# Kernel optimization log

Measured on AMD Instinct MI355X. Metric: run time of the kernel, lower is better.

## Reference

```python
import jax, jax.numpy as jnp
import numpy as np

H = 768; IDX_D = 64; K = 10; R = 12; READ_K = 100; MD = 64; WK = 100; INTER = 3072
SIZES = (100, 1000, 10000, 50000); N = SIZES[-1]; DEPTH = len(SIZES)
B = 4; E = 128
SQ_IDX = np.float32(np.sqrt(IDX_D)); SQ_MD = np.float32(np.sqrt(MD))


def setup_inputs():
    ks = jax.random.split(jax.random.key(0), 16)
    d = {}
    d['elem_hiddens'] = jax.random.normal(ks[0], (B, E, H), jnp.float32)
    d['elems_to_elems'] = 0.05 * jax.random.normal(ks[1], (B, R, E, E), jnp.float32)
    d['Wq_idx'] = jax.random.normal(ks[2], (H, DEPTH * IDX_D), jnp.float32) / np.float32(np.sqrt(H))
    d['bq_idx'] = jnp.zeros((DEPTH * IDX_D,), jnp.float32)
    d['key0'] = 0.01 * jax.random.normal(ks[3], (SIZES[0], IDX_D), jnp.float32)
    d['key1'] = 0.01 * jax.random.normal(ks[4], (SIZES[0], SIZES[1] // SIZES[0], IDX_D), jnp.float32)
    d['key2'] = 0.01 * jax.random.normal(ks[5], (SIZES[1], SIZES[2] // SIZES[1], IDX_D), jnp.float32)
    d['key3'] = 0.01 * jax.random.normal(ks[6], (SIZES[2], SIZES[3] // SIZES[2], IDX_D), jnp.float32)
    d['memory_keys'] = 0.01 * jax.random.normal(ks[7], (R, N, MD), jnp.float32)
    d['memory_values'] = 0.01 * jax.random.normal(ks[8], (R, N, MD), jnp.float32)
    d['wiring_weights'] = jax.random.normal(ks[9], (R, N, WK), jnp.float32)
    d['Wq_mha'] = jax.random.normal(ks[10], (H, R * MD), jnp.float32) / np.float32(np.sqrt(H))
    d['bq_mha'] = jnp.zeros((R * MD,), jnp.float32)
    d['W1'] = jax.random.normal(ks[11], (R * MD, INTER), jnp.float32) / np.float32(np.sqrt(R * MD))
    d['b1'] = jnp.zeros((INTER,), jnp.float32)
    d['W2'] = jax.random.normal(ks[12], (INTER, H), jnp.float32) / np.float32(np.sqrt(INTER))
    d['b2'] = jnp.zeros((H,), jnp.float32)
    d['ln_g'] = jnp.ones((H,), jnp.float32)
    d['ln_b'] = jnp.zeros((H,), jnp.float32)
    d['wiring_edges'] = jax.random.randint(ks[13], (R, N, WK), 0, N, jnp.int32)
    return d


def _indexer(x, Wq, bq, keys):
    # hierarchical product-key top-k retrieval; ind holds node ids at each level
    q = (x @ Wq + bq).reshape(x.shape[:-1] + (DEPTH, IDX_D))
    attn = jax.nn.softmax(jnp.einsum('bed,nd->ben', q[..., 0, :], keys[0]) / SQ_IDX, axis=-1)
    val, ind = jax.lax.top_k(attn, K)
    val = val / val.sum(-1, keepdims=True)
    for i in range(1, DEPTH):
        branch = SIZES[i] // SIZES[i - 1]
        kk = keys[i][ind]  # [B,E,K,branch,D] gather children of surviving nodes
        s = jax.nn.softmax(jnp.einsum('bed,bekcd->bekc', q[..., i, :], kk) / SQ_IDX, axis=-1)
        a = (val[..., None] * s).reshape(x.shape[:-1] + (K * branch,))
        val, f = jax.lax.top_k(a, K)
        ind = jnp.take_along_axis(ind, f // branch, axis=-1) * branch + f % branch
        val = val / val.sum(-1, keepdims=True)
    return val, ind  # [B,E,K] weights, [B,E,K] node ids in [0,N)


def reference(elem_hiddens, elems_to_elems, Wq_idx, bq_idx, key0, key1, key2, key3, memory_keys, memory_values, wiring_weights, Wq_mha, bq_mha, W1, b1, W2, b2, ln_g, ln_b, wiring_edges):
    e2n_val, e2n_ind = _indexer(elem_hiddens, Wq_idx, bq_idx, (key0, key1, key2, key3))
    rows = jnp.arange(B * E)[:, None]
    write_loss = jnp.float32(0.0)
    mem_keys_l, mem_vals_l = [], []
    for r in range(R):
        # sparse-sparse matmul e2n @ n2n realized as gather + scatter-add (coalesces dups like spspmm)
        nbr = wiring_edges[r][e2n_ind]  # [B,E,K,WK]
        w = wiring_weights[r][e2n_ind]  # [B,E,K,WK]
        cand_val = (e2n_val[..., None] * w).reshape(B * E, K * WK)
        cand_col = nbr.reshape(B * E, K * WK)
        e22n = jnp.zeros((B * E, N), jnp.float32).at[rows, cand_col].add(cand_val).reshape(B, E, N)
        # e222e[b,i,j] = sum_a e2n_val[b,j,a] * e22n[b,i,e2n_ind[b,j,a]] (batch-block-diagonal spspmm)
        g = jnp.take_along_axis(e22n[:, :, None, :], e2n_ind[:, None, :, :], axis=-1)  # [B,Ei,Ej,K]
        e222e = jnp.einsum('bijk,bjk->bij', g, e2n_val)
        write_loss = write_loss + jnp.mean((e222e - elems_to_elems[:, r]) ** 2)
        _, top_ind = jax.lax.top_k(e22n, READ_K)  # sparse_topk per row (>=~500 positive nnz per row)
        mem_keys_l += [memory_keys[r][e2n_ind], memory_keys[r][top_ind]]
        mem_vals_l += [memory_values[r][e2n_ind], memory_values[r][top_ind]]
    slots = K + READ_K
    mem_keys = jnp.concatenate(mem_keys_l, axis=2).reshape(B, E, R, slots, MD)
    mem_vals = jnp.concatenate(mem_vals_l, axis=2).reshape(B, E, R, slots, MD)
    # multi-head read; note: original scores queries against VALUES (not keys)
    qh = (elem_hiddens @ Wq_mha + bq_mha).reshape(B, E, R, MD)
    attn = jax.nn.softmax(jnp.einsum('berd,bersd->bers', qh, mem_vals) / SQ_MD, axis=-1)
    attd = jnp.einsum('bers,bersd->berd', attn, mem_vals).reshape(B, E, R * MD)
    h = jax.nn.gelu(attd @ W1 + b1, approximate=False) @ W2 + b2
    mu = h.mean(-1, keepdims=True)
    out = (h - mu) / jnp.sqrt(((h - mu) ** 2).mean(-1, keepdims=True) + 1e-5) * ln_g + ln_b
    return out, write_loss
```

## Files before the change

kernel.cpp:

```cpp
#include <hip/hip_runtime.h>
#include <hip/hip_bf16.h>
#include <cfloat>
#include <cmath>

#define H_DIM 768
#define IDX_D 64
#define KTOP 10
#define R_HEADS 12
#define READ_K 100
#define MD 64
#define WK 100
#define INTER 3072
#define N_NODES 50000
#define B_SZ 4
#define E_SZ 128
#define BE 512
#define SLOTS 110
#define HASH_SZ 2048
#define HASH_MASK 2047

__global__ void zero_loss_kernel(float* p) {
    if (threadIdx.x == 0 && blockIdx.x == 0) *p = 0.f;
}
__global__ void write_loss_kernel(const float* p, float* out) {
    if (threadIdx.x == 0 && blockIdx.x == 0) out[0] = *p / 65536.f;
}

__global__ __launch_bounds__(256) void gemm_kernel(
    const float* __restrict__ A, const float* __restrict__ Bm,
    const float* __restrict__ bias, float* __restrict__ C,
    int M, int N, int K, int act)
{
    __shared__ float As[2][16][65];
    __shared__ float Bs[2][16][65];
    const int tid = threadIdx.x;
    const int tx = tid & 15, ty = tid >> 4;
    const int m0 = blockIdx.y * 64, n0 = blockIdx.x * 64;

    const int aty = tid >> 4, atx = tid & 15;
    const int bky = tid >> 6, bnx = tid & 63;

    float acc[4][4] = {};
    float av[4], bv[4];

    auto stage = [&](int k0) {
        #pragma unroll
        for (int j = 0; j < 4; ++j)
            av[j] = A[(size_t)(m0 + aty + 16 * j) * K + k0 + atx];
        #pragma unroll
        for (int j = 0; j < 4; ++j)
            bv[j] = Bm[(size_t)(k0 + bky + 4 * j) * N + n0 + bnx];
    };
    auto commit = [&](int buf) {
        #pragma unroll
        for (int j = 0; j < 4; ++j) As[buf][atx][aty + 16 * j] = av[j];
        #pragma unroll
        for (int j = 0; j < 4; ++j) Bs[buf][bky + 4 * j][bnx] = bv[j];
    };
    auto compute = [&](int buf) {
        #pragma unroll
        for (int kk = 0; kk < 16; ++kk) {
            float a4[4], b4[4];
            #pragma unroll
            for (int u = 0; u < 4; ++u) a4[u] = As[buf][kk][ty * 4 + u];
            #pragma unroll
            for (int v = 0; v < 4; ++v) b4[v] = Bs[buf][kk][tx * 4 + v];
            #pragma unroll
            for (int u = 0; u < 4; ++u)
                #pragma unroll
                for (int v = 0; v < 4; ++v) acc[u][v] += a4[u] * b4[v];
        }
    };

    stage(0);
    commit(0);
    __syncthreads();
    int buf = 0;
    for (int k0 = 16; k0 < K; k0 += 16) {
        stage(k0);
        compute(buf);
        commit(buf ^ 1);
        __syncthreads();
        buf ^= 1;
    }
    compute(buf);

    #pragma unroll
    for (int u = 0; u < 4; ++u) {
        int m = m0 + ty * 4 + u;
        #pragma unroll
        for (int v = 0; v < 4; ++v) {
            int n = n0 + tx * 4 + v;
            float x = acc[u][v] + bias[n];
            if (act) x = 0.5f * x * (1.f + erff(x * 0.70710678118654752f));
            C[(size_t)m * N + n] = x;
        }
    }
}

typedef short bf16x8 __attribute__((ext_vector_type(8)));
typedef float f32x4 __attribute__((ext_vector_type(4)));
typedef unsigned int u32x4 __attribute__((ext_vector_type(4)));

__device__ inline unsigned f2bf(float x) {
    unsigned u = __float_as_uint(x);
    return (u + 0x7FFFu + ((u >> 16) & 1u)) >> 16;
}
__device__ inline float bfval(unsigned b) { return __uint_as_float(b << 16); }

__global__ __launch_bounds__(256) void gemm_mfma_kernel(
    const float* __restrict__ A, const float* __restrict__ Bm,
    const float* __restrict__ bias, float* __restrict__ C,
    int M, int N, int Kc, int lda, int act)
{
    __shared__ __align__(16) unsigned int lds[2][4][2048];

    const int tid = threadIdx.x;
    const int lane = tid & 63;
    const int w = tid >> 6, wr = w >> 1, wc = w & 1;
    const int m0 = blockIdx.y * 128, n0 = blockIdx.x * 128;
    const int kbase = blockIdx.z * Kc;
    float* __restrict__ Cp = C + (size_t)blockIdx.z * M * N;

    f32x4 acc[4][4] = {};
    unsigned apk[2][8];
    unsigned bpk[2][8];

    auto stage = [&](int k0) {
        #pragma unroll
        for (int it = 0; it < 8; ++it) {
            int idx = it * 256 + tid;
            int r = idx >> 4, p = idx & 15;
            const float2 v = *(const float2*)(A + (size_t)(m0 + r) * lda + kbase + k0 + 2 * p);
            unsigned h0 = f2bf(v.x), h1 = f2bf(v.y);
            apk[0][it] = h0 | (h1 << 16);
            apk[1][it] = f2bf(v.x - bfval(h0)) | (f2bf(v.y - bfval(h1)) << 16);
        }
        #pragma unroll
        for (int it = 0; it < 4; ++it) {
            int idx = it * 256 + tid;
            int cp = idx & 63, kp = idx >> 6;
            const float* bp = Bm + (size_t)(kbase + k0 + 2 * kp) * N + n0 + 2 * cp;
            const float2 e = *(const float2*)bp;
            const float2 o = *(const float2*)(bp + N);
            unsigned he0 = f2bf(e.x), ho0 = f2bf(o.x);
            unsigned he1 = f2bf(e.y), ho1 = f2bf(o.y);
            bpk[0][it * 2 + 0] = he0 | (ho0 << 16);
            bpk[1][it * 2 + 0] = f2bf(e.x - bfval(he0)) | (f2bf(o.x - bfval(ho0)) << 16);
            bpk[0][it * 2 + 1] = he1 | (ho1 << 16);
            bpk[1][it * 2 + 1] = f2bf(e.y - bfval(he1)) | (f2bf(o.y - bfval(ho1)) << 16);
        }
    };

    auto commit = [&](int buf) {
        #pragma unroll
        for (int it = 0; it < 8; ++it) {
            int idx = it * 256 + tid;
            int r = idx >> 4, p = idx & 15;
            int off = ((r >> 4) * 256) + ((p >> 2) * 64) + ((r & 15) * 4) + (p & 3);
            lds[buf][0][off] = apk[0][it];
            lds[buf][1][off] = apk[1][it];
        }
        #pragma unroll
        for (int it = 0; it < 4; ++it) {
            int idx = it * 256 + tid;
            int cp = idx & 63, kp = idx >> 6;
            int c = 2 * cp, g = kp >> 2, jj = kp & 3;
            int off0 = ((c >> 4) * 256) + (g * 64) + ((c & 15) * 4) + jj;
            lds[buf][2][off0]     = bpk[0][it * 2 + 0];
            lds[buf][3][off0]     = bpk[1][it * 2 + 0];
            lds[buf][2][off0 + 4] = bpk[0][it * 2 + 1];
            lds[buf][3][off0 + 4] = bpk[1][it * 2 + 1];
        }
    };

    auto ldfrag = [&](const unsigned* p) -> bf16x8 {
        return __builtin_bit_cast(bf16x8, *(const u32x4*)p);
    };

    auto compute = [&](int buf) {
        bf16x8 ah[4], al[4], bh[4], bl[4];
        #pragma unroll
        for (int mt = 0; mt < 4; ++mt) {
            int sub = wr * 4 + mt;
            ah[mt] = ldfrag(&lds[buf][0][sub * 256 + lane * 4]);
            al[mt] = ldfrag(&lds[buf][1][sub * 256 + lane * 4]);
        }
        #pragma unroll
        for (int nt = 0; nt < 4; ++nt) {
            int sub = wc * 4 + nt;
            bh[nt] = ldfrag(&lds[buf][2][sub * 256 + lane * 4]);
            bl[nt] = ldfrag(&lds[buf][3][sub * 256 + lane * 4]);
        }
        #pragma unroll
        for (int mt = 0; mt < 4; ++mt)
            #pragma unroll
            for (int nt = 0; nt < 4; ++nt) {
                acc[mt][nt] = __builtin_amdgcn_mfma_f32_16x16x32_bf16(ah[mt], bh[nt], acc[mt][nt], 0, 0, 0);
                acc[mt][nt] = __builtin_amdgcn_mfma_f32_16x16x32_bf16(ah[mt], bl[nt], acc[mt][nt], 0, 0, 0);
                acc[mt][nt] = __builtin_amdgcn_mfma_f32_16x16x32_bf16(al[mt], bh[nt], acc[mt][nt], 0, 0, 0);
            }
    };

    stage(0);
    commit(0);
    __syncthreads();
    int buf = 0;
    for (int k0 = 32; k0 < Kc; k0 += 32) {
        stage(k0);
        compute(buf);
        commit(buf ^ 1);
        __syncthreads();
        buf ^= 1;
    }
    compute(buf);

    const int rb0 = (lane >> 4) * 4, cc = lane & 15;
    #pragma unroll
    for (int mt = 0; mt < 4; ++mt) {
        #pragma unroll
        for (int nt = 0; nt < 4; ++nt) {
            int col = n0 + wc * 64 + nt * 16 + cc;
            int row = m0 + wr * 64 + mt * 16 + rb0;
            float b = bias ? bias[col] : 0.f;
            #pragma unroll
            for (int reg = 0; reg < 4; ++reg) {
                float x = acc[mt][nt][reg] + b;
                if (act) x = 0.5f * x * (1.f + erff(x * 0.70710678118654752f));
                Cp[(size_t)(row + reg) * N + col] = x;
            }
        }
    }
}

__device__ inline void wave_topk10(volatile float* a, int cnt,
                                   float* vnew, int* inew, int t)
{
    for (int iter = 0; iter < 10; ++iter) {
        float bv = -FLT_MAX;
        int bi = 0x7fffffff;
        for (int n = t; n < cnt; n += 64) {
            float v = a[n];
            if (v > bv) { bv = v; bi = n; }
        }
        #pragma unroll
        for (int off = 32; off; off >>= 1) {
            float ov = __shfl_xor(bv, off, 64);
            int   oi = __shfl_xor(bi, off, 64);
            if (ov > bv || (ov == bv && oi < bi)) { bv = ov; bi = oi; }
        }
        if (t == 0) { vnew[iter] = bv; inew[iter] = bi; a[bi] = -FLT_MAX; }
        __syncthreads();
    }
}

__global__ __launch_bounds__(64) void indexer_kernel(
    const float* __restrict__ qidx,
    const float* __restrict__ key0,
    const float* __restrict__ key1,
    const float* __restrict__ key2,
    const float* __restrict__ key3,
    float* __restrict__ e2n_val,
    int* __restrict__ e2n_ind)
{
    const int be = blockIdx.x;
    const int t = threadIdx.x;
    __shared__ float q[256];
    __shared__ float sraw[100];
    __shared__ float a[100];
    __shared__ float vnew[10]; __shared__ int inew[10];
    __shared__ float vcur[10]; __shared__ int icur[10];
    __shared__ float km[10], ks[10];

    for (int idx = t; idx < 256; idx += 64) q[idx] = qidx[(size_t)be * 256 + idx];
    __syncthreads();

    for (int n = t; n < 100; n += 64) {
        float dot = 0.f;
        const float* kp = key0 + (size_t)n * 64;
        #pragma unroll 8
        for (int d = 0; d < 64; ++d) dot += q[d] * kp[d];
        sraw[n] = dot * 0.125f;
    }
    __syncthreads();
    float lm = -FLT_MAX;
    for (int n = t; n < 100; n += 64) lm = fmaxf(lm, sraw[n]);
    #pragma unroll
    for (int off = 32; off; off >>= 1) lm = fmaxf(lm, __shfl_xor(lm, off, 64));
    float lsum = 0.f;
    for (int n = t; n < 100; n += 64) { float e = expf(sraw[n] - lm); a[n] = e; lsum += e; }
    #pragma unroll
    for (int off = 32; off; off >>= 1) lsum += __shfl_xor(lsum, off, 64);
    __syncthreads();
    for (int n = t; n < 100; n += 64) a[n] /= lsum;
    __syncthreads();
    wave_topk10(a, 100, vnew, inew, t);
    if (t == 0) {
        float s = 0.f;
        for (int u = 0; u < 10; ++u) s += vnew[u];
        for (int u = 0; u < 10; ++u) { vcur[u] = vnew[u] / s; icur[u] = inew[u]; }
    }
    __syncthreads();

    for (int lvl = 1; lvl < 4; ++lvl) {
        const int br = (lvl < 3) ? 10 : 5;
        const float* kb = (lvl == 1) ? key1 : ((lvl == 2) ? key2 : key3);
        const int cnt = 10 * br;
        const float* qv = q + lvl * 64;
        for (int c = t; c < cnt; c += 64) {
            int k = c / br, cc = c - k * br;
            const float* kp = kb + ((size_t)icur[k] * br + cc) * 64;
            float dot = 0.f;
            #pragma unroll 8
            for (int d = 0; d < 64; ++d) dot += qv[d] * kp[d];
            sraw[c] = dot * 0.125f;
        }
        __syncthreads();
        if (t < 10) {
            float m = -FLT_MAX;
            for (int cc = 0; cc < br; ++cc) m = fmaxf(m, sraw[t * br + cc]);
            float s = 0.f;
            for (int cc = 0; cc < br; ++cc) s += expf(sraw[t * br + cc] - m);
            km[t] = m; ks[t] = s;
        }
        __syncthreads();
        for (int c = t; c < cnt; c += 64) {
            int k = c / br;
            a[c] = vcur[k] * expf(sraw[c] - km[k]) / ks[k];
        }
        __syncthreads();
        wave_topk10(a, cnt, vnew, inew, t);
        if (t == 0) {
            float s = 0.f;
            for (int u = 0; u < 10; ++u) s += vnew[u];
            int ni[10]; float nv[10];
            for (int u = 0; u < 10; ++u) {
                int f = inew[u];
                ni[u] = icur[f / br] * br + (f % br);
                nv[u] = vnew[u] / s;
            }
            for (int u = 0; u < 10; ++u) { icur[u] = ni[u]; vcur[u] = nv[u]; }
        }
        __syncthreads();
    }
    if (t < 10) {
        e2n_val[(size_t)be * 10 + t] = vcur[t];
        e2n_ind[(size_t)be * 10 + t] = icur[t];
    }
}

__global__ __launch_bounds__(256) void scatter_loss_topk_kernel(
    const int* __restrict__ e2n_ind,
    const float* __restrict__ e2n_val,
    const int* __restrict__ edges,
    const float* __restrict__ wts,
    const float* __restrict__ e2e,
    int* __restrict__ top_ind,
    float* __restrict__ loss_acc)
{
    __shared__ int   hkey[HASH_SZ];
    __shared__ float hval[HASH_SZ];
    __shared__ int   pool[2560];
    __shared__ float red[256];
    __shared__ int   chunkSuf[256];
    __shared__ int   s_t, s_above, s_cntA, s_cntB;

    const int blk = blockIdx.x;
    const int r = blk >> 9;
    const int be = blk & 511;
    const int b = be >> 7, i = be & 127;
    const int tid = threadIdx.x;

    int* s_ind = pool;
    float* s_val = (float*)(pool + 1280);

    for (int idx = tid; idx < E_SZ * KTOP; idx += 256) {
        s_ind[idx] = e2n_ind[(size_t)b * E_SZ * KTOP + idx];
        s_val[idx] = e2n_val[(size_t)b * E_SZ * KTOP + idx];
    }
    for (int idx = tid; idx < HASH_SZ; idx += 256) { hkey[idx] = -1; hval[idx] = 0.f; }
    if (tid == 0) { s_t = -1; s_above = 0; s_cntA = 0; s_cntB = 0; }
    __syncthreads();

    const size_t rbase = (size_t)r * N_NODES * WK;
    for (int c = tid; c < KTOP * WK; c += 256) {
        int k = c / WK, wk = c - k * WK;
        int node = s_ind[i * KTOP + k];
        float v0 = s_val[i * KTOP + k];
        size_t off = rbase + (size_t)node * WK + wk;
        int col = edges[off];
        float v = v0 * wts[off];
        unsigned h = ((unsigned)col * 2654435761u) >> 21;
        for (;;) {
            int old = atomicCAS(&hkey[h], -1, col);
            if (old == -1 || old == col) { atomicAdd(&hval[h], v); break; }
            h = (h + 1) & HASH_MASK;
        }
    }
    __syncthreads();

    {
        const int j = tid & 127, half = tid >> 7;
        float acc = 0.f;
        #pragma unroll
        for (int k = half * 5; k < half * 5 + 5; ++k) {
            int col = s_ind[j * KTOP + k];
            float vv = s_val[j * KTOP + k];
            unsigned h = ((unsigned)col * 2654435761u) >> 21;
            float g = 0.f;
            for (;;) {
                int kk = hkey[h];
                if (kk == col) { g = hval[h]; break; }
                if (kk == -1) break;
                h = (h + 1) & HASH_MASK;
            }
            acc += vv * g;
        }
        red[tid] = acc;
        __syncthreads();
        float sq = 0.f;
        if (tid < 128) {
            float tot = red[tid] + red[tid + 128];
            float d = tot - e2e[(((size_t)b * R_HEADS + r) * E_SZ + i) * E_SZ + tid];
            sq = d * d;
        }
        __syncthreads();
        red[tid] = sq;
        __syncthreads();
        for (int off = 128; off; off >>= 1) {
            if (tid < off) red[tid] += red[tid + off];
            __syncthreads();
        }
        if (tid == 0) atomicAdd(loss_acc, red[0]);
    }
    __syncthreads();

    int* hist = pool;
    for (int idx = tid; idx < HASH_SZ; idx += 256) hist[idx] = 0;
    __syncthreads();
    for (int idx = tid; idx < HASH_SZ; idx += 256) {
        float v = hval[idx];
        if (hkey[idx] != -1 && v > 0.f)
            atomicAdd(&hist[(__float_as_uint(v) >> 20) & 0x7FF], 1);
    }
    __syncthreads();
    {
        int csum = 0;
        #pragma unroll
        for (int bb = 0; bb < 8; ++bb) csum += hist[tid * 8 + bb];
        chunkSuf[tid] = csum;
    }
    __syncthreads();
    if (tid == 0) {
        int suf = 0;
        for (int c = 255; c >= 0; --c) { int t0 = chunkSuf[c]; chunkSuf[c] = suf; suf += t0; }
    }
    __syncthreads();
    {
        int cum = chunkSuf[tid];
        for (int bb = tid * 8 + 7; bb >= tid * 8; --bb) {
            int h = hist[bb];
            if (cum < READ_K && cum + h >= READ_K) { s_t = bb; s_above = cum; }
            cum += h;
        }
    }
    __syncthreads();
    const int tbin = s_t;

    int* bcol = pool;
    float* bval = (float*)(pool + 1024);
    __syncthreads();
    int* outp = top_ind + ((size_t)be * R_HEADS + r) * READ_K;
    for (int idx = tid; idx < HASH_SZ; idx += 256) {
        float v = hval[idx];
        if (hkey[idx] == -1 || v <= 0.f) continue;
        int bin = (__float_as_uint(v) >> 20) & 0x7FF;
        if (bin > tbin) {
            int p = atomicAdd(&s_cntA, 1);
            if (p < READ_K) outp[p] = hkey[idx];
        } else if (bin == tbin) {
            int p = atomicAdd(&s_cntB, 1);
            bcol[p] = hkey[idx]; bval[p] = v;
        }
    }
    __syncthreads();
    const int above = s_cntA;
    const int m = s_cntB;
    int rem = READ_K - above;
    if (rem >= m) {
        for (int idx = tid; idx < m; idx += 256) outp[above + idx] = bcol[idx];
        for (int idx = above + m + tid; idx < READ_K; idx += 256) outp[idx] = 0;
    } else if (tid < 64) {
        volatile float* bv_ = bval;
        for (int it = 0; it < rem; ++it) {
            float bvx = -FLT_MAX; int bi = -1;
            for (int n = tid; n < m; n += 64) {
                float v = bv_[n];
                if (v > bvx) { bvx = v; bi = n; }
            }
            #pragma unroll
            for (int off = 32; off; off >>= 1) {
                float ov = __shfl_xor(bvx, off, 64);
                int   oi = __shfl_xor(bi, off, 64);
                if (ov > bvx) { bvx = ov; bi = oi; }
            }
            if (tid == 0) { outp[above + it] = bcol[bi]; bv_[bi] = -FLT_MAX; }
        }
    }
}

__global__ __launch_bounds__(128) void attn_kernel(
    const float* __restrict__ qh,
    const int* __restrict__ e2n_ind,
    const int* __restrict__ top_ind,
    const float* __restrict__ memv,
    float* __restrict__ attd)
{
    __shared__ float vv[SLOTS * 65];
    __shared__ int slots[SLOTS];
    __shared__ float qv[64];
    __shared__ float sc[SLOTS];
    __shared__ float red[128];

    const int blk = blockIdx.x;
    const int r = blk >> 9, be = blk & 511;
    const int tid = threadIdx.x;

    if (tid < KTOP) slots[tid] = e2n_ind[(size_t)be * KTOP + tid];
    else if (tid < SLOTS) slots[tid] = top_ind[((size_t)be * R_HEADS + r) * READ_K + (tid - KTOP)];
    if (tid < 64) qv[tid] = qh[(size_t)be * H_DIM + r * 64 + tid];
    __syncthreads();

    const size_t rb = (size_t)r * N_NODES * 64;
    for (int idx = tid; idx < SLOTS * 64; idx += 128) {
        int s = idx >> 6, d = idx & 63;
        vv[s * 65 + d] = memv[rb + (size_t)slots[s] * 64 + d];
    }
    __syncthreads();

    if (tid < SLOTS) {
        float dot = 0.f;
        const float* vp = vv + tid * 65;
        #pragma unroll 8
        for (int d = 0; d < 64; ++d) dot += qv[d] * vp[d];
        sc[tid] = dot * 0.125f;
    }
    __syncthreads();

    red[tid] = (tid < SLOTS) ? sc[tid] : -FLT_MAX;
    __syncthreads();
    for (int off = 64; off; off >>= 1) {
        if (tid < off) red[tid] = fmaxf(red[tid], red[tid + off]);
        __syncthreads();
    }
    float m = red[0];
    __syncthreads();
    float e = (tid < SLOTS) ? expf(sc[tid] - m) : 0.f;
    red[tid] = e;
    __syncthreads();
    for (int off = 64; off; off >>= 1) {
        if (tid < off) red[tid] += red[tid + off];
        __syncthreads();
    }
    float sum = red[0];
    if (tid < SLOTS) sc[tid] = e / sum;
    __syncthreads();

    {
        const int d = tid & 63;
        const int s0 = (tid >> 6) * 55;
        float acc = 0.f;
        for (int s = s0; s < s0 + 55; ++s) acc += sc[s] * vv[s * 65 + d];
        red[tid] = acc;
        __syncthreads();
        if (tid < 64)
            attd[(size_t)be * H_DIM + r * 64 + tid] = red[tid] + red[tid + 64];
    }
}

__global__ __launch_bounds__(256) void ln_kernel(
    const float* __restrict__ hp,
    const float* __restrict__ b2,
    const float* __restrict__ g,
    const float* __restrict__ bta, float* __restrict__ out)
{
    const int be = blockIdx.x, tid = threadIdx.x;
    __shared__ float red[256];
    const size_t st = (size_t)BE * H_DIM;
    const size_t base = (size_t)be * 768;
    float x0 = b2[tid], x1 = b2[tid + 256], x2 = b2[tid + 512];
    #pragma unroll
    for (int s = 0; s < 4; ++s) {
        x0 += hp[s * st + base + tid];
        x1 += hp[s * st + base + 256 + tid];
        x2 += hp[s * st + base + 512 + tid];
    }
    red[tid] = x0 + x1 + x2;
    __syncthreads();
    for (int off = 128; off; off >>= 1) { if (tid < off) red[tid] += red[tid + off]; __syncthreads(); }
    const float mu = red[0] * (1.f / 768.f);
    __syncthreads();
    const float d0 = x0 - mu, d1 = x1 - mu, d2 = x2 - mu;
    red[tid] = d0 * d0 + d1 * d1 + d2 * d2;
    __syncthreads();
    for (int off = 128; off; off >>= 1) { if (tid < off) red[tid] += red[tid + off]; __syncthreads(); }
    const float rstd = rsqrtf(red[0] * (1.f / 768.f) + 1e-5f);
    out[(size_t)be * 768 + tid]       = d0 * rstd * g[tid]       + bta[tid];
    out[(size_t)be * 768 + 256 + tid] = d1 * rstd * g[tid + 256] + bta[tid + 256];
    out[(size_t)be * 768 + 512 + tid] = d2 * rstd * g[tid + 512] + bta[tid + 512];
}

extern "C" void kernel_launch(void* const* d_in, const int* in_sizes, int n_in,
                              void* d_out, int out_size, void* d_ws, size_t ws_size,
                              hipStream_t stream)
{
    const float* elem_hiddens = (const float*)d_in[0];
    const float* e2e          = (const float*)d_in[1];
    const float* Wq_idx       = (const float*)d_in[2];
    const float* bq_idx       = (const float*)d_in[3];
    const float* key0         = (const float*)d_in[4];
    const float* key1         = (const float*)d_in[5];
    const float* key2         = (const float*)d_in[6];
    const float* key3         = (const float*)d_in[7];
    const float* memv         = (const float*)d_in[9];
    const float* wir_w        = (const float*)d_in[10];
    const float* Wq_mha       = (const float*)d_in[11];
    const float* bq_mha       = (const float*)d_in[12];
    const float* W1           = (const float*)d_in[13];
    const float* b1           = (const float*)d_in[14];
    const float* W2           = (const float*)d_in[15];
    const float* b2           = (const float*)d_in[16];
    const float* ln_g         = (const float*)d_in[17];
    const float* ln_b         = (const float*)d_in[18];
    const int*   wir_e        = (const int*)d_in[19];
    float* out = (float*)d_out;

    char* ws = (char*)d_ws;
    float* loss    = (float*)ws;
    float* q_idx   = (float*)(ws + 256);
    float* qh      = q_idx + (size_t)BE * 256;
    float* e2n_val = qh + (size_t)BE * H_DIM;
    int*   e2n_ind = (int*)(e2n_val + BE * KTOP);
    int*   top_ind = e2n_ind + BE * KTOP;
    float* attd    = (float*)(top_ind + (size_t)BE * R_HEADS * READ_K);
    float* h1      = attd + (size_t)BE * H_DIM;
    float* h2p     = h1 + (size_t)BE * INTER;

    zero_loss_kernel<<<1, 64, 0, stream>>>(loss);

    gemm_kernel<<<dim3(256 / 64, BE / 64), 256, 0, stream>>>(
        elem_hiddens, Wq_idx, bq_idx, q_idx, BE, 256, H_DIM, 0);
    gemm_mfma_kernel<<<dim3(H_DIM / 128, BE / 128, 1), 256, 0, stream>>>(
        elem_hiddens, Wq_mha, bq_mha, qh, BE, H_DIM, H_DIM, H_DIM, 0);

    indexer_kernel<<<BE, 64, 0, stream>>>(q_idx, key0, key1, key2, key3,
                                          e2n_val, e2n_ind);

    scatter_loss_topk_kernel<<<R_HEADS * BE, 256, 0, stream>>>(
        e2n_ind, e2n_val, wir_e, wir_w, e2e, top_ind, loss);

    attn_kernel<<<R_HEADS * BE, 128, 0, stream>>>(qh, e2n_ind, top_ind, memv, attd);

    gemm_mfma_kernel<<<dim3(INTER / 128, BE / 128, 1), 256, 0, stream>>>(
        attd, W1, b1, h1, BE, INTER, H_DIM, H_DIM, 1);
    gemm_mfma_kernel<<<dim3(H_DIM / 128, BE / 128, 4), 256, 0, stream>>>(
        h1, W2, nullptr, h2p, BE, H_DIM, INTER / 4, INTER, 0);

    ln_kernel<<<BE, 256, 0, stream>>>(h2p, b2, ln_g, ln_b, out);
    write_loss_kernel<<<1, 64, 0, stream>>>(loss, out + (size_t)BE * H_DIM);
}
```

Measured before the change: 1.055 ms.

## Vectorize dot products, prefetch edges, use wave-shuffle reductions across kernels

The indexer uses float4 vectorized 64-wide dot products. The scatter kernel no longer stages the whole batch's e2n arrays in shared memory: each thread's gathered edges and weights are issued up front into registers, the neighbor lookups read global memory directly, and the block reductions and suffix scan become wave shuffles. The attention kernel moves to 256 threads, gathers with float4 loads and replaces tree reductions with shuffle reductions. These changes target latency from gather loads and syncthreads, at the cost of more register pressure and cached global reads in place of shared-memory reads.

Result: faster. 1.015 ms (-3.7%).

```diff
diff --git a/kernel.cpp b/kernel.cpp
--- a/kernel.cpp
+++ b/kernel.cpp
@@ -254,6 +254,24 @@
     }
 }
 
+__device__ inline float dot64_seq(const float* __restrict__ qv,
+                                  const float* __restrict__ kp)
+{
+    const float4* k4 = (const float4*)kp;
+    const float4* q4 = (const float4*)qv;
+    float dot = 0.f;
+    #pragma unroll
+    for (int d4 = 0; d4 < 16; ++d4) {
+        float4 kv = k4[d4];
+        float4 qq = q4[d4];
+        dot += qq.x * kv.x;
+        dot += qq.y * kv.y;
+        dot += qq.z * kv.z;
+        dot += qq.w * kv.w;
+    }
+    return dot;
+}
+
 __global__ __launch_bounds__(64) void indexer_kernel(
     const float* __restrict__ qidx,
     const float* __restrict__ key0,
@@ -265,7 +283,7 @@
 {
     const int be = blockIdx.x;
     const int t = threadIdx.x;
-    __shared__ float q[256];
+    __shared__ __align__(16) float q[256];
     __shared__ float sraw[100];
     __shared__ float a[100];
     __shared__ float vnew[10]; __shared__ int inew[10];
@@ -276,11 +294,7 @@
     __syncthreads();
 
     for (int n = t; n < 100; n += 64) {
-        float dot = 0.f;
-        const float* kp = key0 + (size_t)n * 64;
-        #pragma unroll 8
-        for (int d = 0; d < 64; ++d) dot += q[d] * kp[d];
-        sraw[n] = dot * 0.125f;
+        sraw[n] = dot64_seq(q, key0 + (size_t)n * 64) * 0.125f;
     }
     __syncthreads();
     float lm = -FLT_MAX;
@@ -310,10 +324,7 @@
         for (int c = t; c < cnt; c += 64) {
             int k = c / br, cc = c - k * br;
             const float* kp = kb + ((size_t)icur[k] * br + cc) * 64;
-            float dot = 0.f;
-            #pragma unroll 8
-            for (int d = 0; d < 64; ++d) dot += qv[d] * kp[d];
-            sraw[c] = dot * 0.125f;
+            sraw[c] = dot64_seq(qv, kp) * 0.125f;
         }
         __syncthreads();
         if (t < 10) {
@@ -360,52 +371,74 @@
 {
     __shared__ int   hkey[HASH_SZ];
     __shared__ float hval[HASH_SZ];
-    __shared__ int   pool[2560];
-    __shared__ float red[256];
-    __shared__ int   chunkSuf[256];
-    __shared__ int   s_t, s_above, s_cntA, s_cntB;
+    __shared__ int   pool[HASH_SZ];
+    __shared__ float red[128];
+    __shared__ float wred[4];
+    __shared__ int   sufw[4];
+    __shared__ int   s_t, s_cntA, s_cntB;
 
     const int blk = blockIdx.x;
     const int r = blk >> 9;
     const int be = blk & 511;
     const int b = be >> 7, i = be & 127;
     const int tid = threadIdx.x;
-
-    int* s_ind = pool;
-    float* s_val = (float*)(pool + 1280);
-
-    for (int idx = tid; idx < E_SZ * KTOP; idx += 256) {
-        s_ind[idx] = e2n_ind[(size_t)b * E_SZ * KTOP + idx];
-        s_val[idx] = e2n_val[(size_t)b * E_SZ * KTOP + idx];
+    const int lane = tid & 63, wid = tid >> 6;
+
+    const size_t rbase = (size_t)r * N_NODES * WK;
+    const int be10 = be * KTOP;
+    int col0, col1, col2, col3 = -2;
+    float val0, val1, val2, val3 = 0.f;
+    {
+        int c = tid, k = c / WK, wk = c - k * WK;
+        int node = e2n_ind[be10 + k]; float v0 = e2n_val[be10 + k];
+        size_t off = rbase + (size_t)node * WK + wk;
+        col0 = edges[off]; val0 = v0 * wts[off];
+    }
+    {
+        int c = tid + 256, k = c / WK, wk = c - k * WK;
+        int node = e2n_ind[be10 + k]; float v0 = e2n_val[be10 + k];
+        size_t off = rbase + (size_t)node * WK + wk;
+        col1 = edges[off]; val1 = v0 * wts[off];
+    }
+    {
+        int c = tid + 512, k = c / WK, wk = c - k * WK;
+        int node = e2n_ind[be10 + k]; float v0 = e2n_val[be10 + k];
+        size_t off = rbase + (size_t)node * WK + wk;
+        col2 = edges[off]; val2 = v0 * wts[off];
+    }
+    const bool has3 = (tid + 768) < KTOP * WK;
+    if (has3) {
+        int c = tid + 768, k = c / WK, wk = c - k * WK;
+        int node = e2n_ind[be10 + k]; float v0 = e2n_val[be10 + k];
+        size_t off = rbase + (size_t)node * WK + wk;
+        col3 = edges[off]; val3 = v0 * wts[off];
     }
     for (int idx = tid; idx < HASH_SZ; idx += 256) { hkey[idx] = -1; hval[idx] = 0.f; }
-    if (tid == 0) { s_t = -1; s_above = 0; s_cntA = 0; s_cntB = 0; }
-    __syncthreads();
-
-    const size_t rbase = (size_t)r * N_NODES * WK;
-    for (int c = tid; c < KTOP * WK; c += 256) {
-        int k = c / WK, wk = c - k * WK;
-        int node = s_ind[i * KTOP + k];
-        float v0 = s_val[i * KTOP + k];
-        size_t off = rbase + (size_t)node * WK + wk;
-        int col = edges[off];
-        float v = v0 * wts[off];
+    if (tid == 0) { s_t = -1; s_cntA = 0; s_cntB = 0; }
+    __syncthreads();
+
+    auto insert = [&](int col, float v) {
         unsigned h = ((unsigned)col * 2654435761u) >> 21;
         for (;;) {
             int old = atomicCAS(&hkey[h], -1, col);
             if (old == -1 || old == col) { atomicAdd(&hval[h], v); break; }
             h = (h + 1) & HASH_MASK;
         }
-    }
+    };
+    insert(col0, val0);
+    insert(col1, val1);
+    insert(col2, val2);
+    if (has3) insert(col3, val3);
     __syncthreads();
 
     {
         const int j = tid & 127, half = tid >> 7;
+        const int jb = (b * E_SZ + j) * KTOP;
         float acc = 0.f;
         #pragma unroll
         for (int k = half * 5; k < half * 5 + 5; ++k) {
-            int col = s_ind[j * KTOP + k];
-            float vv = s_val[j * KTOP + k];
+            int col = e2n_ind[jb + k];
+            float vv = e2n_val[jb + k];
             unsigned h = ((unsigned)col * 2654435761u) >> 21;
             float g = 0.f;
             for (;;) {
@@ -416,24 +449,20 @@
             }
             acc += vv * g;
         }
-        red[tid] = acc;
+        if (half == 0) red[j] = acc;
         __syncthreads();
         float sq = 0.f;
-        if (tid < 128) {
-            float tot = red[tid] + red[tid + 128];
-            float d = tot - e2e[(((size_t)b * R_HEADS + r) * E_SZ + i) * E_SZ + tid];
+        if (half == 1) {
+            float tot = red[j] + acc;
+            float d = tot - e2e[(((size_t)b * R_HEADS + r) * E_SZ + i) * E_SZ + j];
             sq = d * d;
         }
-        __syncthreads();
-        red[tid] = sq;
-        __syncthreads();
-        for (int off = 128; off; off >>= 1) {
-            if (tid < off) red[tid] += red[tid + off];
-            __syncthreads();
-        }
-        if (tid == 0) atomicAdd(loss_acc, red[0]);
-    }
-    __syncthreads();
+        #pragma unroll
+        for (int off = 32; off; off >>= 1) sq += __shfl_xor(sq, off, 64);
+        if (lane == 0) wred[wid] = sq;
+        __syncthreads();
+        if (tid == 0) atomicAdd(loss_acc, wred[0] + wred[1] + wred[2] + wred[3]);
+    }
 
     int* hist = pool;
     for (int idx = tid; idx < HASH_SZ; idx += 256) hist[idx] = 0;
@@ -444,23 +473,25 @@
             atomicAdd(&hist[(__float_as_uint(v) >> 20) & 0x7FF], 1);
     }
     __syncthreads();
+
     {
         int csum = 0;
         #pragma unroll
         for (int bb = 0; bb < 8; ++bb) csum += hist[tid * 8 + bb];
-        chunkSuf[tid] = csum;
-    }
-    __syncthreads();
-    if (tid == 0) {
-        int suf = 0;
-        for (int c = 255; c >= 0; --c) { int t0 = chunkSuf[c]; chunkSuf[c] = suf; suf += t0; }
-    }
-    __syncthreads();
-    {
-        int cum = chunkSuf[tid];
+        int cincl = csum;
+        #pragma unroll
+        for (int st = 1; st < 64; st <<= 1) {
+            int o = __shfl_down(cincl, st, 64);
+            if (lane + st < 64) cincl += o;
+        }
+        if (lane == 0) sufw[wid] = cincl;
+        __syncthreads();
+        int aboveW = 0;
+        for (int ww = wid + 1; ww < 4; ++ww) aboveW += sufw[ww];
+        int cum = aboveW + (cincl - csum);
         for (int bb = tid * 8 + 7; bb >= tid * 8; --bb) {
             int h = hist[bb];
-            if (cum < READ_K && cum + h >= READ_K) { s_t = bb; s_above = cum; }
+            if (cum < READ_K && cum + h >= READ_K) s_t = bb;
             cum += h;
         }
     }
@@ -469,7 +500,6 @@
 
     int* bcol = pool;
     float* bval = (float*)(pool + 1024);
-    __syncthreads();
     int* outp = top_ind + ((size_t)be * R_HEADS + r) * READ_K;
     for (int idx = tid; idx < HASH_SZ; idx += 256) {
         float v = hval[idx];
@@ -509,7 +539,7 @@
     }
 }
 
-__global__ __launch_bounds__(128) void attn_kernel(
+__global__ __launch_bounds__(256) void attn_kernel(
     const float* __restrict__ qh,
     const int* __restrict__ e2n_ind,
     const int* __restrict__ top_ind,
@@ -520,21 +550,24 @@
     __shared__ int slots[SLOTS];
     __shared__ float qv[64];
     __shared__ float sc[SLOTS];
-    __shared__ float red[128];
+    __shared__ float red[256];
 
     const int blk = blockIdx.x;
     const int r = blk >> 9, be = blk & 511;
     const int tid = threadIdx.x;
+    const int lane = tid & 63, wid = tid >> 6;
 
     if (tid < KTOP) slots[tid] = e2n_ind[(size_t)be * KTOP + tid];
     else if (tid < SLOTS) slots[tid] = top_ind[((size_t)be * R_HEADS + r) * READ_K + (tid - KTOP)];
     if (tid < 64) qv[tid] = qh[(size_t)be * H_DIM + r * 64 + tid];
     __syncthreads();
 
-    const size_t rb = (size_t)r * N_NODES * 64;
-    for (int idx = tid; idx < SLOTS * 64; idx += 128) {
-        int s = idx >> 6, d = idx & 63;
-        vv[s * 65 + d] = memv[rb + (size_t)slots[s] * 64 + d];
+    const float4* mv4 = (const float4*)(memv + (size_t)r * N_NODES * 64);
+    for (int idx = tid; idx < SLOTS * 16; idx += 256) {
+        int s = idx >> 4, q4 = idx & 15;
+        float4 v = mv4[(size_t)slots[s] * 16 + q4];
+        float* dst = vv + s * 65 + q4 * 4;
+        dst[0] = v.x; dst[1] = v.y; dst[2] = v.z; dst[3] = v.w;
     }
     __syncthreads();
 
@@ -547,34 +580,31 @@
     }
     __syncthreads();
 
-    red[tid] = (tid < SLOTS) ? sc[tid] : -FLT_MAX;
-    __syncthreads();
-    for (int off = 64; off; off >>= 1) {
-        if (tid < off) red[tid] = fmaxf(red[tid], red[tid + off]);
-        __syncthreads();
-    }
-    float m = red[0];
-    __syncthreads();
-    float e = (tid < SLOTS) ? expf(sc[tid] - m) : 0.f;
-    red[tid] = e;
-    __syncthreads();
-    for (int off = 64; off; off >>= 1) {
-        if (tid < off) red[tid] += red[tid + off];
-        __syncthreads();
-    }
-    float sum = red[0];
+    float v = (tid < SLOTS) ? sc[tid] : -FLT_MAX;
+    #pragma unroll
+    for (int off = 32; off; off >>= 1) v = fmaxf(v, __shfl_xor(v, off, 64));
+    if (lane == 0) red[wid] = v;
+    __syncthreads();
+    const float mx = fmaxf(fmaxf(red[0], red[1]), fmaxf(red[2], red[3]));
+    float e = (tid < SLOTS) ? expf(sc[tid] - mx) : 0.f;
+    float s = e;
+    #pragma unroll
+    for (int off = 32; off; off >>= 1) s += __shfl_xor(s, off, 64);
+    if (lane == 0) red[4 + wid] = s;
+    __syncthreads();
+    const float sum = red[4] + red[5] + red[6] + red[7];
     if (tid < SLOTS) sc[tid] = e / sum;
     __syncthreads();
 
     {
         const int d = tid & 63;
-        const int s0 = (tid >> 6) * 55;
         float acc = 0.f;
-        for (int s = s0; s < s0 + 55; ++s) acc += sc[s] * vv[s * 65 + d];
+        for (int ss = wid; ss < SLOTS; ss += 4) acc += sc[ss] * vv[ss * 65 + d];
         red[tid] = acc;
         __syncthreads();
         if (tid < 64)
-            attd[(size_t)be * H_DIM + r * 64 + tid] = red[tid] + red[tid + 64];
+            attd[(size_t)be * H_DIM + r * 64 + tid] =
+                red[tid] + red[tid + 64] + red[tid + 128] + red[tid + 192];
     }
 }
 
@@ -659,7 +689,7 @@
     scatter_loss_topk_kernel<<<R_HEADS * BE, 256, 0, stream>>>(
         e2n_ind, e2n_val, wir_e, wir_w, e2e, top_ind, loss);
 
-    attn_kernel<<<R_HEADS * BE, 128, 0, stream>>>(qh, e2n_ind, top_ind, memv, attd);
+    attn_kernel<<<R_HEADS * BE, 256, 0, stream>>>(qh, e2n_ind, top_ind, memv, attd);
 
     gemm_mfma_kernel<<<dim3(INTER / 128, BE / 128, 1), 256, 0, stream>>>(
         attd, W1, b1, h1, BE, INTER, H_DIM, H_DIM, 1);
```
